# Optimization experiments

Measured on AMD Instinct MI355X. Metric: run time of the kernel, lower is better.

The kernel has to match this reference:

```python
import jax, jax.numpy as jnp
import numpy as np
from jax import lax

NUM_ITER = 20
STOP_THRESH = 1e-4
# kernels baked from anisotropy=(1,1,0.5): (3,3,3) and (max(1,int(3*s)),...)=(3,3,1)
KERNELS = ((3, 3, 3), (3, 3, 1))
LEAK = 0.01


def _maxpool3d(x, k):
    # x: [B,C,D,H,W]; stride 1, torch-style padding (k-1)//2 (pads with -inf for max)
    window = (1, 1) + k
    pad = [(0, 0), (0, 0)] + [((ki - 1) // 2, (ki - 1) // 2) for ki in k]
    return lax.reduce_window(x, -jnp.inf, lax.max, window, (1,) * 5, pad)


def soft_erode(img):
    p = [-_maxpool3d(-img, k) for k in KERNELS]
    return jnp.minimum(p[0], p[1])


def soft_dilate(img):
    p = [_maxpool3d(img, k) for k in KERNELS]
    return jnp.maximum(p[0], p[1])


def soft_open(img):
    return soft_dilate(soft_erode(img))


def _leaky(x):
    return jax.nn.leaky_relu(x, LEAK)


def soft_skel(img):
    skel = _leaky(img - soft_open(img))
    prev_skel = jnp.zeros_like(skel)
    active = jnp.array(True)  # emulates the data-dependent `break`
    for i in range(NUM_ITER):
        img = soft_erode(img)
        lr = 0.1 * 0.5 ** (i // (NUM_ITER // 5))
        delta = _leaky(img - soft_open(img))
        skel_update = _leaky(delta - skel * delta) * lr
        skel_new = skel + skel_update
        delta_norm = jnp.mean(jnp.abs(skel_new - prev_skel))
        # torch updates skel, THEN checks and breaks; freeze after stop triggers
        skel = jnp.where(active, skel_new, skel)
        active = jnp.logical_and(active, delta_norm >= STOP_THRESH)
        prev_skel = skel
    return skel


def distance_transform(x):
    binary = (x > 0).astype(x.dtype)
    return -1.0 * (1.0 - binary) * _maxpool3d(-binary, (3, 3, 3))


def setup_inputs() -> dict:
    key = jax.random.key(0)
    img = jax.random.uniform(key, (2, 1, 128, 256, 256), dtype=jnp.float32)
    return {"img": img}


def reference(img):
    skel = soft_skel(img)
    dt = distance_transform(lax.stop_gradient(skel))  # mirrors skel.detach()
    return skel * (1.0 + 0.2 * jax.nn.sigmoid(dt))
```

## Files before the change

kernel.cpp:

```cpp
#include <hip/hip_runtime.h>
#include <hip/hip_cooperative_groups.h>
#include <cmath>

#define D_ 128
#define H_ 256
#define W4 64
#define PS (H_*W4)
#define NTOT (2*128*256*256)
#define GBLK 2048
#define ROWS 8
#define TSTART 6
#define STOPF 1e-4f

typedef _Float16 h4 __attribute__((ext_vector_type(4)));
typedef _Float16 h2v __attribute__((ext_vector_type(2)));

__device__ __forceinline__ float lk(float x){ return x >= 0.f ? x : 0.01f*x; }
__device__ __forceinline__ float4 mn4(float4 a, float4 b){
    return make_float4(fminf(a.x,b.x),fminf(a.y,b.y),fminf(a.z,b.z),fminf(a.w,b.w)); }
__device__ __forceinline__ float4 ld4(const float4* p){ return *p; }
__device__ __forceinline__ float4 ld4(const h4* p){
    h4 v = *p; return make_float4((float)v.x,(float)v.y,(float)v.z,(float)v.w); }
__device__ __forceinline__ void st4(h4* p, float4 v){
    h4 r; r.x=(_Float16)v.x; r.y=(_Float16)v.y; r.z=(_Float16)v.z; r.w=(_Float16)v.w; *p = r; }
__device__ __forceinline__ float4 h4tof4(h4 v){
    return make_float4((float)v.x,(float)v.y,(float)v.z,(float)v.w); }

#define PINF 0x7C007C00u
#define NINF 0xFC00FC00u
__device__ __forceinline__ uint32_t pmin(uint32_t a, uint32_t b){
    h2v r = __builtin_elementwise_min(__builtin_bit_cast(h2v,a), __builtin_bit_cast(h2v,b));
    return __builtin_bit_cast(uint32_t, r); }
__device__ __forceinline__ uint32_t pmax(uint32_t a, uint32_t b){
    h2v r = __builtin_elementwise_max(__builtin_bit_cast(h2v,a), __builtin_bit_cast(h2v,b));
    return __builtin_bit_cast(uint32_t, r); }
__device__ __forceinline__ uint2 pmin2(uint2 a, uint2 b){
    return make_uint2(pmin(a.x,b.x), pmin(a.y,b.y)); }
__device__ __forceinline__ uint2 pmax2(uint2 a, uint2 b){
    return make_uint2(pmax(a.x,b.x), pmax(a.y,b.y)); }
__device__ __forceinline__ float4 cvt4(uint32_t w01, uint32_t w23){
    h2v a = __builtin_bit_cast(h2v, w01);
    h2v b = __builtin_bit_cast(h2v, w23);
    return make_float4((float)a.x, (float)a.y, (float)b.x, (float)b.y); }

struct Geo { int lane, h0; size_t pbase; bool pm, pp; };
__device__ __forceinline__ Geo mkgeo(int tid, int bi){
    Geo g;
    g.lane = tid & 63;
    int wv = tid >> 6;
    int q = bi & 7, d = (bi >> 3) & 127, b = bi >> 10;
    g.h0 = q*32 + wv*ROWS;
    g.pbase = ((size_t)(b*128 + d))*PS + (size_t)g.lane;
    g.pm = (d > 0); g.pp = (d < 127);
    return g;
}

__device__ __forceinline__ void phase_f32_erode(
    const float4* __restrict__ Xm, const float4* __restrict__ Xc, const float4* __restrict__ Xp,
    bool pm, bool pp, h4* __restrict__ Ep, int h0, int lane)
{
    const float INF = __builtin_inff();
    float4 dmn[4];
    auto ldrow = [&](int j){
        int s = j & 3; int h = h0 - 1 + j;
        if (h >= 0 && h < H_){
            float4 v = ld4(Xc + h*W4); float4 mn = v;
            if (pm){ mn = mn4(mn, ld4(Xm + h*W4)); }
            if (pp){ mn = mn4(mn, ld4(Xp + h*W4)); }
            dmn[s] = mn;
        } else dmn[s] = make_float4(INF,INF,INF,INF);
    };
    ldrow(0); ldrow(1); ldrow(2);
#pragma unroll
    for (int r = 0; r < ROWS; ++r){
        if (r + 3 <= ROWS + 1) ldrow(r+3);
        float4 vmn = mn4(dmn[r&3], mn4(dmn[(r+1)&3], dmn[(r+2)&3]));
        float lmn = __shfl_up(vmn.w,1);   if (lane == 0)  lmn = INF;
        float rmn = __shfl_down(vmn.x,1); if (lane == 63) rmn = INF;
        float4 e;
        e.x = fminf(lmn,  fminf(vmn.x,vmn.y));
        e.y = fminf(vmn.x,fminf(vmn.y,vmn.z));
        e.z = fminf(vmn.y,fminf(vmn.z,vmn.w));
        e.w = fminf(vmn.z,fminf(vmn.w,rmn));
        st4(Ep + (h0+r)*W4, e);
    }
}

template<int MODE, int R, typename CT>
__device__ __forceinline__ double phase_pk(
    const uint2* __restrict__ Xm, const uint2* __restrict__ Xc, const uint2* __restrict__ Xp,
    bool pm, bool pp,
    uint2* __restrict__ Ep, const CT* __restrict__ Cp, h4* __restrict__ Sp,
    float lr, int h0, int lane)
{
    uint2 rmn[4], rmx[4];
    double loc = 0.0;
    auto ldrow = [&](int j){
        int s = j & 3; int h = h0 - 1 + j;
        if (h >= 0 && h < H_){
            uint2 v = *(Xc + h*W4); uint2 mn = v, mx = v;
            if (pm){ uint2 u = *(Xm + h*W4); mn = pmin2(mn,u); mx = pmax2(mx,u); }
            if (pp){ uint2 u = *(Xp + h*W4); mn = pmin2(mn,u); mx = pmax2(mx,u); }
            rmn[s] = mn; rmx[s] = mx;
        } else {
            rmn[s] = make_uint2(PINF,PINF);
            rmx[s] = make_uint2(NINF,NINF);
        }
    };
    ldrow(0); ldrow(1); ldrow(2);
    float4 a_cur = ld4(Cp + h0*W4);
    float4 s_cur = make_float4(0,0,0,0);
    if constexpr(MODE >= 2) s_cur = ld4(Sp + h0*W4);
#pragma unroll
    for (int r = 0; r < R; ++r){
        if (r + 3 <= R + 1) ldrow(r+3);
        float4 a_nxt = a_cur, s_nxt = s_cur;
        if (r + 1 < R){
            a_nxt = ld4(Cp + (h0+r+1)*W4);
            if constexpr(MODE >= 2) s_nxt = ld4(Sp + (h0+r+1)*W4);
        }
        uint2 vmn = pmin2(rmn[r&3], pmin2(rmn[(r+1)&3], rmn[(r+2)&3]));
        uint2 vmx = pmax2(rmx[r&3], pmax2(rmx[(r+1)&3], rmx[(r+2)&3]));
        uint32_t pwn = __shfl_up(vmn.y,1);   if (lane == 0)  pwn = PINF;
        uint32_t nwn = __shfl_down(vmn.x,1); if (lane == 63) nwn = PINF;
        uint32_t l01 = (pwn  >> 16) | (vmn.x << 16);
        uint32_t l23 = (vmn.x >> 16) | (vmn.y << 16);
        uint32_t r23 = (vmn.y >> 16) | (nwn  << 16);
        uint32_t e01 = pmin(pmin(l01, vmn.x), l23);
        uint32_t e23 = pmin(pmin(l23, vmn.y), r23);
        *(Ep + (h0+r)*W4) = make_uint2(e01, e23);
        uint32_t pwx = __shfl_up(vmx.y,1);   if (lane == 0)  pwx = NINF;
        uint32_t nwx = __shfl_down(vmx.x,1); if (lane == 63) nwx = NINF;
        uint32_t L01 = (pwx  >> 16) | (vmx.x << 16);
        uint32_t L23 = (vmx.x >> 16) | (vmx.y << 16);
        uint32_t R23 = (vmx.y >> 16) | (nwx  << 16);
        uint32_t o01 = pmax(pmax(L01, vmx.x), L23);
        uint32_t o23 = pmax(pmax(L23, vmx.y), R23);
        float4 o = cvt4(o01, o23);
        float4 a = a_cur;
        if constexpr(MODE == 1){
            float4 s0;
            s0.x = lk(a.x-o.x); s0.y = lk(a.y-o.y);
            s0.z = lk(a.z-o.z); s0.w = lk(a.w-o.w);
            st4(Sp + (h0+r)*W4, s0);
        } else {
            float4 s = s_cur;
            float4 up; float dl;
            dl = lk(a.x-o.x); up.x = lk(dl - s.x*dl)*lr; s.x += up.x;
            dl = lk(a.y-o.y); up.y = lk(dl - s.y*dl)*lr; s.y += up.y;
            dl = lk(a.z-o.z); up.z = lk(dl - s.z*dl)*lr; s.z += up.z;
            dl = lk(a.w-o.w); up.w = lk(dl - s.w*dl)*lr; s.w += up.w;
            st4(Sp + (h0+r)*W4, s);
            if constexpr(MODE == 2)
                loc += (double)(fabsf(s.x)+fabsf(s.y)+fabsf(s.z)+fabsf(s.w));
            else
                loc += (double)(fabsf(up.x)+fabsf(up.y)+fabsf(up.z)+fabsf(up.w));
        }
        a_cur = a_nxt; s_cur = s_nxt;
    }
    return loc;
}

__global__ __launch_bounds__(256) void p0_k(const float* __restrict__ img0,
                                            h4* __restrict__ R0,
                                            int* __restrict__ frozen){
    if (blockIdx.x == 0 && threadIdx.x == 0) *frozen = 0;
    Geo g = mkgeo(threadIdx.x, blockIdx.x);
    const float4* Xc = (const float4*)img0 + g.pbase;
    phase_f32_erode(Xc-PS, Xc, Xc+PS, g.pm, g.pp, R0+g.pbase, g.h0, g.lane);
}

__global__ __launch_bounds__(256) void p1_k(const h4* __restrict__ R0,
                                            const float* __restrict__ img0,
                                            h4* __restrict__ R1,
                                            h4* __restrict__ S){
    Geo g = mkgeo(threadIdx.x, blockIdx.x);
    const uint2* Xc = (const uint2*)R0 + g.pbase;
    phase_pk<1,ROWS,float4>(Xc-PS, Xc, Xc+PS, g.pm, g.pp, (uint2*)R1 + g.pbase,
                            (const float4*)img0 + g.pbase, S + g.pbase, 0.f, g.h0, g.lane);
}

template<int MODE>
__global__ __launch_bounds__(256) void upd_k(const h4* __restrict__ Xb,
                                             const h4* __restrict__ Cb,
                                             h4* __restrict__ Eb,
                                             h4* __restrict__ Sb,
                                             const double* __restrict__ pr,
                                             double* __restrict__ pw,
                                             int* __restrict__ frozen,
                                             float* __restrict__ outp,
                                             float lr){
    if (*frozen) return;
    __shared__ double sm[4];
    int tid = threadIdx.x;
    int lane = tid & 63, wv = tid >> 6;
    if constexpr(MODE == 3){
        double v = 0.0;
#pragma unroll
        for (int j = 0; j < GBLK/256; ++j) v += pr[tid + 256*j];
#pragma unroll
        for (int o = 32; o; o >>= 1) v += __shfl_down(v, o);
        if (lane == 0) sm[wv] = v;
        __syncthreads();
        double tot = sm[0] + sm[1] + sm[2] + sm[3];
        if ((float)(tot / (double)NTOT) < STOPF){
            if (tid == 0) *frozen = 1;
            Geo g = mkgeo(tid, blockIdx.x);
            const h4* Sp = Sb + g.pbase;
            float4* O = (float4*)outp + g.pbase;
#pragma unroll
            for (int r = 0; r < ROWS; ++r){
                float4 s = h4tof4(Sp[(g.h0+r)*W4]);
                O[(g.h0+r)*W4] = make_float4(1.1f*s.x, 1.1f*s.y, 1.1f*s.z, 1.1f*s.w);
            }
            return;
        }
        __syncthreads();
    }
    Geo g = mkgeo(tid, blockIdx.x);
    const uint2* Xc = (const uint2*)Xb + g.pbase;
    double loc = phase_pk<MODE,ROWS,h4>(Xc-PS, Xc, Xc+PS, g.pm, g.pp,
                                        (uint2*)Eb + g.pbase, Cb + g.pbase, Sb + g.pbase,
                                        lr, g.h0, g.lane);
#pragma unroll
    for (int o = 32; o; o >>= 1) loc += __shfl_down(loc, o);
    if (lane == 0) sm[wv] = loc;
    __syncthreads();
    if (tid == 0) pw[blockIdx.x] = sm[0]+sm[1]+sm[2]+sm[3];
}

__global__ __launch_bounds__(256) void tail_k(h4* __restrict__ rg0,
                                              h4* __restrict__ rg1,
                                              h4* __restrict__ rg2,
                                              h4* __restrict__ S,
                                              float* __restrict__ outp,
                                              const double* __restrict__ pr0,
                                              double* __restrict__ tp0,
                                              double* __restrict__ tp1,
                                              const int* __restrict__ frozen){
    if (*frozen) return;
    cooperative_groups::grid_group gg = cooperative_groups::this_grid();
    __shared__ double sm[4];
    int tid = threadIdx.x, lane = tid & 63, wv = tid >> 6;
    int bi = blockIdx.x;
    int d = bi >> 3, b = (bi >> 2) & 1, q = bi & 3;
    int h0 = q*64 + wv*16;
    size_t pbase = ((size_t)(b*128 + d))*PS + (size_t)lane;
    bool pm = d > 0, pp = d < 127;
    const double* pr = pr0; int prn = GBLK;
    double* tpw = tp0;
    for (int i = TSTART; i < 20; ++i){
        double v = 0.0;
        for (int j = 0; j < prn/256; ++j) v += pr[tid + 256*j];
#pragma unroll
        for (int o = 32; o; o >>= 1) v += __shfl_down(v, o);
        if (lane == 0) sm[wv] = v;
        __syncthreads();
        double tot = sm[0] + sm[1] + sm[2] + sm[3];
        if ((float)(tot / (double)NTOT) < STOPF) break;
        __syncthreads();
        int xs = (i+1)%3, es = (i+2)%3, cs = i%3;
        h4* X = xs==0 ? rg0 : (xs==1 ? rg1 : rg2);
        h4* E = es==0 ? rg0 : (es==1 ? rg1 : rg2);
        h4* C = cs==0 ? rg0 : (cs==1 ? rg1 : rg2);
        float lr = 0.1f * exp2f(-(float)(i >> 2));
        const uint2* Xc = (const uint2*)X + pbase;
        double loc = phase_pk<3,16,h4>(Xc-PS, Xc, Xc+PS, pm, pp, (uint2*)E + pbase,
                                       C + pbase, S + pbase, lr, h0, lane);
#pragma unroll
        for (int o = 32; o; o >>= 1) loc += __shfl_down(loc, o);
        if (lane == 0) sm[wv] = loc;
        __syncthreads();
        if (tid == 0) tpw[blockIdx.x] = sm[0]+sm[1]+sm[2]+sm[3];
        gg.sync();
        pr = tpw; prn = 1024;
        tpw = (tpw == tp0) ? tp1 : tp0;
    }
    const h4* Sp = S + pbase;
    float4* O = (float4*)outp + pbase;
#pragma unroll
    for (int r = 0; r < 16; ++r){
        float4 s = h4tof4(Sp[(h0+r)*W4]);
        O[(h0+r)*W4] = make_float4(1.1f*s.x, 1.1f*s.y, 1.1f*s.z, 1.1f*s.w);
    }
}

__global__ __launch_bounds__(256) void scale_k(const h4* __restrict__ S,
                                               float* __restrict__ out){
    int t = blockIdx.x*256 + threadIdx.x;
#pragma unroll
    for (int c = 0; c < 4; ++c){
        int i = t + c*1048576;
        float4 s = ld4(S + i);
        float4 r = make_float4(1.1f*s.x, 1.1f*s.y, 1.1f*s.z, 1.1f*s.w);
        *(float4*)(out + (size_t)i*4) = r;
    }
}

extern "C" void kernel_launch(void* const* d_in, const int* in_sizes, int n_in,
                              void* d_out, int out_size, void* d_ws, size_t ws_size,
                              hipStream_t stream){
    const float* img0 = (const float*)d_in[0];
    float* out = (float*)d_out;
    char* ws = (char*)d_ws;
    size_t volh = (size_t)NTOT * 2;
    h4* ring[3] = { (h4*)ws, (h4*)(ws + volh), (h4*)(ws + 2*volh) };
    h4* S       = (h4*)(ws + 3*volh);
    double* parts[2] = { (double*)(ws + 4*volh), (double*)(ws + 4*volh) + GBLK };
    int* frozen = (int*)(ws + 4*volh + 2*GBLK*sizeof(double));
    double* tp0 = (double*)(ws + 4*volh + 2*GBLK*sizeof(double) + 256);
    double* tp1 = tp0 + 1024;

    dim3 blk(256), grd(GBLK);
    hipLaunchKernelGGL(p0_k, grd, blk, 0, stream, img0, ring[0], frozen);
    hipLaunchKernelGGL(p1_k, grd, blk, 0, stream, ring[0], img0, ring[1], S);

    for (int i = 0; i < TSTART; ++i){
        h4* C = ring[i % 3];
        h4* X = ring[(i+1) % 3];
        h4* E = ring[(i+2) % 3];
        float lr = (float)(0.1 * pow(0.5, (double)(i / 4)));
        double* pw = parts[i & 1];
        double* pr = parts[1 - (i & 1)];
        if (i == 0)
            hipLaunchKernelGGL((upd_k<2>), grd, blk, 0, stream, X, C, E, S, pr, pw, frozen, out, lr);
        else
            hipLaunchKernelGGL((upd_k<3>), grd, blk, 0, stream, X, C, E, S, pr, pw, frozen, out, lr);
    }

    h4* a_r0 = ring[0]; h4* a_r1 = ring[1]; h4* a_r2 = ring[2];
    h4* a_S = S; float* a_out = out;
    const double* a_pr0 = parts[1 - (TSTART & 1)];
    double* a_tp0 = tp0; double* a_tp1 = tp1; int* a_fz = frozen;
    void* args[9] = { &a_r0, &a_r1, &a_r2, &a_S, &a_out, &a_pr0, &a_tp0, &a_tp1, &a_fz };
    hipError_t ce = hipLaunchCooperativeKernel((const void*)tail_k, dim3(1024), blk,
                                               args, 0u, stream);
    if (ce != hipSuccess){
        for (int i = TSTART; i < 20; ++i){
            h4* C = ring[i % 3];
            h4* X = ring[(i+1) % 3];
            h4* E = ring[(i+2) % 3];
            float lr = (float)(0.1 * pow(0.5, (double)(i / 4)));
            double* pw = parts[i & 1];
            double* pr = parts[1 - (i & 1)];
            hipLaunchKernelGGL((upd_k<3>), grd, blk, 0, stream, X, C, E, S, pr, pw, frozen, out, lr);
        }
        hipLaunchKernelGGL(scale_k, dim3(4096), blk, 0, stream, S, out);
    }
}
```

Baseline: 289.7 us.

## Fuse two skeleton iterations per kernel with a two-level erosion stencil

Adds a new path in which each kernel advances two soft-skeleton iterations. It computes the second erosion and both opens from a depth-extended neighbourhood (d±2) loaded once, which roughly halves the number of launches and full-volume passes. Convergence norms are checked one pair late using per-iteration partial buffers, and the previous skeleton is kept so the output can come from the correct iterate. In exchange it does more redundant stencil work per pass, needs extra workspace, and only runs when the workspace is large enough; otherwise it falls back to the old cooperative path.

```diff
diff --git a/kernel.cpp b/kernel.cpp
--- a/kernel.cpp
+++ b/kernel.cpp
@@ -25,6 +25,8 @@
     h4 r; r.x=(_Float16)v.x; r.y=(_Float16)v.y; r.z=(_Float16)v.z; r.w=(_Float16)v.w; *p = r; }
 __device__ __forceinline__ float4 h4tof4(h4 v){
     return make_float4((float)v.x,(float)v.y,(float)v.z,(float)v.w); }
+__device__ __forceinline__ h4 f4toh4(float4 v){
+    h4 r; r.x=(_Float16)v.x; r.y=(_Float16)v.y; r.z=(_Float16)v.z; r.w=(_Float16)v.w; return r; }
 
 #define PINF 0x7C007C00u
 #define NINF 0xFC00FC00u
@@ -42,6 +44,25 @@
     h2v a = __builtin_bit_cast(h2v, w01);
     h2v b = __builtin_bit_cast(h2v, w23);
     return make_float4((float)a.x, (float)a.y, (float)b.x, (float)b.y); }
+__device__ __forceinline__ uint2 pk4(float4 v){
+    return __builtin_bit_cast(uint2, f4toh4(v)); }
+
+__device__ __forceinline__ uint2 hmin2(uint2 v, int lane){
+    uint32_t pw = __shfl_up(v.y,1);   if (lane == 0)  pw = PINF;
+    uint32_t nw = __shfl_down(v.x,1); if (lane == 63) nw = PINF;
+    uint32_t l01 = (pw  >> 16) | (v.x << 16);
+    uint32_t l23 = (v.x >> 16) | (v.y << 16);
+    uint32_t r23 = (v.y >> 16) | (nw  << 16);
+    return make_uint2(pmin(pmin(l01,v.x),l23), pmin(pmin(l23,v.y),r23));
+}
+__device__ __forceinline__ uint2 hmax2(uint2 v, int lane){
+    uint32_t pw = __shfl_up(v.y,1);   if (lane == 0)  pw = NINF;
+    uint32_t nw = __shfl_down(v.x,1); if (lane == 63) nw = NINF;
+    uint32_t l01 = (pw  >> 16) | (v.x << 16);
+    uint32_t l23 = (v.x >> 16) | (v.y << 16);
+    uint32_t r23 = (v.y >> 16) | (nw  << 16);
+    return make_uint2(pmax(pmax(l01,v.x),l23), pmax(pmax(l23,v.y),r23));
+}
 
 struct Geo { int lane, h0; size_t pbase; bool pm, pp; };
 __device__ __forceinline__ Geo mkgeo(int tid, int bi){
@@ -53,6 +74,267 @@
     g.pbase = ((size_t)(b*128 + d))*PS + (size_t)g.lane;
     g.pm = (d > 0); g.pp = (d < 127);
     return g;
+}
+
+__global__ __launch_bounds__(256) void init_k(const float* __restrict__ img0,
+                                              h4* __restrict__ R0,
+                                              h4* __restrict__ R1,
+                                              h4* __restrict__ Sb,
+                                              int* __restrict__ frozen){
+    if (blockIdx.x == 0 && threadIdx.x == 0) *frozen = 0;
+    int tid = threadIdx.x, lane = tid & 63, wv = tid >> 6;
+    int bi = blockIdx.x;
+    int q = bi & 7, d = (bi >> 3) & 127, b = bi >> 10;
+    int h0 = q*32 + wv*8;
+    size_t pbase = ((size_t)(b*128 + d))*PS + (size_t)lane;
+    bool dm1 = d >= 1, dm2 = d >= 2, dp1 = d <= 126, dp2 = d <= 125;
+    const float4* Xc = (const float4*)img0 + pbase;
+    uint2* E1w = (uint2*)R0 + pbase;
+    uint2* E2w = (uint2*)R1 + pbase;
+    h4*    Sw  = Sb + pbase;
+
+    float4 rawC[4];
+    uint2 mnA[4], mnB[4], mnC[4], mnE[4], mxE[4];
+
+    auto ldmg = [&](int h, int sl){
+        if (h >= 0 && h < H_){
+            const float4* p = Xc + h*W4;
+            float4 c4 = p[0]; rawC[sl] = c4;
+            uint2 c = pk4(c4);
+            uint2 xm1, xm2, xp1, xp2;
+            if (dm1) xm1 = pk4(p[-(int)PS]);
+            if (dm2) xm2 = pk4(p[-2*(int)PS]);
+            if (dp1) xp1 = pk4(p[(int)PS]);
+            if (dp2) xp2 = pk4(p[2*(int)PS]);
+            uint2 mb = c;
+            if (dm1) mb = pmin2(mb, xm1);
+            if (dp1) mb = pmin2(mb, xp1);
+            mnB[sl] = mb;
+            if (dm1){ uint2 a = pmin2(xm1, c); if (dm2) a = pmin2(a, xm2); mnA[sl] = a; }
+            if (dp1){ uint2 cc = pmin2(xp1, c); if (dp2) cc = pmin2(cc, xp2); mnC[sl] = cc; }
+        } else {
+            mnA[sl] = make_uint2(PINF,PINF); mnB[sl] = make_uint2(PINF,PINF);
+            mnC[sl] = make_uint2(PINF,PINF);
+            rawC[sl] = make_float4(0,0,0,0);
+        }
+    };
+    auto e1row = [&](int e, int s0, int s1, int s2, int se, bool wr){
+        if (e >= 0 && e < H_){
+            uint2 vb = pmin2(mnB[s0], pmin2(mnB[s1], mnB[s2]));
+            uint2 e1b = hmin2(vb, lane);
+            uint2 mn = e1b, mx = e1b;
+            if (dm1){
+                uint2 va = pmin2(mnA[s0], pmin2(mnA[s1], mnA[s2]));
+                uint2 e1a = hmin2(va, lane);
+                mn = pmin2(mn, e1a); mx = pmax2(mx, e1a);
+            }
+            if (dp1){
+                uint2 vc = pmin2(mnC[s0], pmin2(mnC[s1], mnC[s2]));
+                uint2 e1c = hmin2(vc, lane);
+                mn = pmin2(mn, e1c); mx = pmax2(mx, e1c);
+            }
+            mnE[se] = mn; mxE[se] = mx;
+            if (wr) E1w[e*W4] = e1b;
+        } else { mnE[se] = make_uint2(PINF,PINF); mxE[se] = make_uint2(NINF,NINF); }
+    };
+
+    ldmg(h0-2, 2); ldmg(h0-1, 3); ldmg(h0+0, 0); ldmg(h0+1, 1);
+    e1row(h0-1, 2,3,0, 3, false);
+    e1row(h0+0, 3,0,1, 0, true);
+#pragma unroll
+    for (int rr = 0; rr < 8; ++rr){
+        int r = h0 + rr;
+        ldmg(r+2, (rr+2)&3);
+        e1row(r+1, rr&3, (rr+1)&3, (rr+2)&3, (rr+1)&3, rr < 7);
+        uint2 v2 = pmin2(mnE[(rr+3)&3], pmin2(mnE[rr&3], mnE[(rr+1)&3]));
+        E2w[r*W4] = hmin2(v2, lane);
+        uint2 vv = pmax2(mxE[(rr+3)&3], pmax2(mxE[rr&3], mxE[(rr+1)&3]));
+        uint2 ow = hmax2(vv, lane);
+        float4 o = cvt4(ow.x, ow.y);
+        float4 a = rawC[rr&3];
+        float4 s0;
+        s0.x = lk(a.x-o.x); s0.y = lk(a.y-o.y);
+        s0.z = lk(a.z-o.z); s0.w = lk(a.w-o.w);
+        st4(Sw + r*W4, s0);
+    }
+}
+
+template<bool FIRST, bool P0>
+__global__ __launch_bounds__(256) void pair_k(const h4* __restrict__ Xb,
+                                              h4* CE1,
+                                              h4* __restrict__ E2b,
+                                              h4* __restrict__ Sb,
+                                              h4* __restrict__ Spb,
+                                              double* __restrict__ nA,
+                                              double* __restrict__ nB,
+                                              const double* __restrict__ g2,
+                                              const double* __restrict__ g1,
+                                              int* __restrict__ frozen,
+                                              float* __restrict__ outp,
+                                              float lr0, float lr1){
+    if (*frozen) return;
+    __shared__ double s2w[4], s1w[4], smA[4], smB[4];
+    int tid = threadIdx.x, lane = tid & 63, wv = tid >> 6;
+    int bi = blockIdx.x;
+    int q = bi & 7, d = (bi >> 3) & 127, b = bi >> 10;
+    int h0 = q*32 + wv*8;
+    size_t pbase = ((size_t)(b*128 + d))*PS + (size_t)lane;
+    if constexpr(!P0){
+        double v2 = 0.0, v1 = 0.0;
+#pragma unroll
+        for (int j = 0; j < GBLK/256; ++j){ v2 += g2[tid + 256*j]; v1 += g1[tid + 256*j]; }
+#pragma unroll
+        for (int o = 32; o; o >>= 1){ v2 += __shfl_down(v2,o); v1 += __shfl_down(v1,o); }
+        if (lane == 0){ s2w[wv] = v2; s1w[wv] = v1; }
+        __syncthreads();
+        double t2 = s2w[0]+s2w[1]+s2w[2]+s2w[3];
+        double t1 = s1w[0]+s1w[1]+s1w[2]+s1w[3];
+        bool f2 = (float)(t2 / (double)NTOT) < STOPF;
+        bool f1 = (float)(t1 / (double)NTOT) < STOPF;
+        if (f2 || f1){
+            if (tid == 0) *frozen = 1;
+            const h4* Sf = (f2 ? Spb : Sb) + pbase;
+            float4* O = (float4*)outp + pbase;
+#pragma unroll
+            for (int r = 0; r < 8; ++r){
+                float4 s = h4tof4(Sf[(h0+r)*W4]);
+                O[(h0+r)*W4] = make_float4(1.1f*s.x, 1.1f*s.y, 1.1f*s.z, 1.1f*s.w);
+            }
+            return;
+        }
+    }
+    bool dm1 = d >= 1, dm2 = d >= 2, dp1 = d <= 126, dp2 = d <= 125;
+    const uint2* Xc = (const uint2*)Xb + pbase;
+    const uint2* Cr = (const uint2*)CE1 + pbase;
+    uint2*       E1w = (uint2*)CE1 + pbase;
+    uint2*       E2w = (uint2*)E2b + pbase;
+    const uint2* Sr  = (const uint2*)Sb + pbase;
+    uint2*       Sw  = (uint2*)Sb + pbase;
+    uint2*       Spw = (uint2*)Spb + pbase;
+
+    uint2 rawC[4], mnA[4], mnB[4], mnC[4], mxB[4], mnE[4], mxE[4];
+    auto ldmg = [&](int h, int sl){
+        if (h >= 0 && h < H_){
+            const uint2* p = Xc + h*W4;
+            uint2 c = p[0]; rawC[sl] = c;
+            uint2 xm1, xm2, xp1, xp2;
+            if (dm1) xm1 = p[-(int)PS];
+            if (dm2) xm2 = p[-2*(int)PS];
+            if (dp1) xp1 = p[(int)PS];
+            if (dp2) xp2 = p[2*(int)PS];
+            uint2 mb = c, xb = c;
+            if (dm1){ mb = pmin2(mb, xm1); xb = pmax2(xb, xm1); }
+            if (dp1){ mb = pmin2(mb, xp1); xb = pmax2(xb, xp1); }
+            mnB[sl] = mb; mxB[sl] = xb;
+            if (dm1){ uint2 a = pmin2(xm1, c); if (dm2) a = pmin2(a, xm2); mnA[sl] = a; }
+            if (dp1){ uint2 cc = pmin2(xp1, c); if (dp2) cc = pmin2(cc, xp2); mnC[sl] = cc; }
+        } else {
+            mnA[sl] = make_uint2(PINF,PINF); mnB[sl] = make_uint2(PINF,PINF);
+            mnC[sl] = make_uint2(PINF,PINF); mxB[sl] = make_uint2(NINF,NINF);
+            rawC[sl] = make_uint2(0,0);
+        }
+    };
+    auto e1row = [&](int e, int s0, int s1, int s2, int se, bool wr){
+        if (e >= 0 && e < H_){
+            uint2 vb = pmin2(mnB[s0], pmin2(mnB[s1], mnB[s2]));
+            uint2 e1b = hmin2(vb, lane);
+            uint2 mn = e1b, mx = e1b;
+            if (dm1){
+                uint2 va = pmin2(mnA[s0], pmin2(mnA[s1], mnA[s2]));
+                uint2 e1a = hmin2(va, lane);
+                mn = pmin2(mn, e1a); mx = pmax2(mx, e1a);
+            }
+            if (dp1){
+                uint2 vc = pmin2(mnC[s0], pmin2(mnC[s1], mnC[s2]));
+                uint2 e1c = hmin2(vc, lane);
+                mn = pmin2(mn, e1c); mx = pmax2(mx, e1c);
+            }
+            mnE[se] = mn; mxE[se] = mx;
+            if (wr) E1w[e*W4] = e1b;
+        } else { mnE[se] = make_uint2(PINF,PINF); mxE[se] = make_uint2(NINF,NINF); }
+    };
+
+    ldmg(h0-2, 2); ldmg(h0-1, 3); ldmg(h0+0, 0); ldmg(h0+1, 1);
+    uint2 cw_cur = Cr[h0*W4];
+    uint2 s_cur  = Sr[h0*W4];
+    e1row(h0-1, 2,3,0, 3, false);
+    e1row(h0+0, 3,0,1, 0, true);
+    double locA = 0.0, locB = 0.0;
+#pragma unroll
+    for (int rr = 0; rr < 8; ++rr){
+        int r = h0 + rr;
+        uint2 cw_nxt = cw_cur, s_nxt = s_cur;
+        if (rr < 7){
+            cw_nxt = Cr[(r+1)*W4];
+            s_nxt  = Sr[(r+1)*W4];
+        }
+        ldmg(r+2, (rr+2)&3);
+        e1row(r+1, rr&3, (rr+1)&3, (rr+2)&3, (rr+1)&3, rr < 7);
+        uint2 v2 = pmin2(mnE[(rr+3)&3], pmin2(mnE[rr&3], mnE[(rr+1)&3]));
+        E2w[r*W4] = hmin2(v2, lane);
+        uint2 vv = pmax2(mxE[(rr+3)&3], pmax2(mxE[rr&3], mxE[(rr+1)&3]));
+        uint2 ovw = hmax2(vv, lane);
+        uint2 vi = pmax2(mxB[(rr+3)&3], pmax2(mxB[rr&3], mxB[(rr+1)&3]));
+        uint2 oiw = hmax2(vi, lane);
+        float4 o = cvt4(oiw.x, oiw.y);
+        float4 a = cvt4(cw_cur.x, cw_cur.y);
+        float4 s = cvt4(s_cur.x, s_cur.y);
+        float4 up; float dl;
+        dl = lk(a.x-o.x); up.x = lk(dl - s.x*dl)*lr0; s.x += up.x;
+        dl = lk(a.y-o.y); up.y = lk(dl - s.y*dl)*lr0; s.y += up.y;
+        dl = lk(a.z-o.z); up.z = lk(dl - s.z*dl)*lr0; s.z += up.z;
+        dl = lk(a.w-o.w); up.w = lk(dl - s.w*dl)*lr0; s.w += up.w;
+        if constexpr(FIRST)
+            locA += (double)(fabsf(s.x)+fabsf(s.y)+fabsf(s.z)+fabsf(s.w));
+        else
+            locA += (double)(fabsf(up.x)+fabsf(up.y)+fabsf(up.z)+fabsf(up.w));
+        h4 s1h = f4toh4(s);
+        Spw[r*W4] = __builtin_bit_cast(uint2, s1h);
+        float4 s2 = h4tof4(s1h);
+        float4 o1 = cvt4(ovw.x, ovw.y);
+        float4 a1 = cvt4(rawC[rr&3].x, rawC[rr&3].y);
+        dl = lk(a1.x-o1.x); up.x = lk(dl - s2.x*dl)*lr1; s2.x += up.x;
+        dl = lk(a1.y-o1.y); up.y = lk(dl - s2.y*dl)*lr1; s2.y += up.y;
+        dl = lk(a1.z-o1.z); up.z = lk(dl - s2.z*dl)*lr1; s2.z += up.z;
+        dl = lk(a1.w-o1.w); up.w = lk(dl - s2.w*dl)*lr1; s2.w += up.w;
+        locB += (double)(fabsf(up.x)+fabsf(up.y)+fabsf(up.z)+fabsf(up.w));
+        Sw[r*W4] = __builtin_bit_cast(uint2, f4toh4(s2));
+        cw_cur = cw_nxt; s_cur = s_nxt;
+    }
+#pragma unroll
+    for (int o = 32; o; o >>= 1){ locA += __shfl_down(locA,o); locB += __shfl_down(locB,o); }
+    if (lane == 0){ smA[wv] = locA; smB[wv] = locB; }
+    __syncthreads();
+    if (tid == 0){
+        nA[bi] = smA[0]+smA[1]+smA[2]+smA[3];
+        nB[bi] = smB[0]+smB[1]+smB[2]+smB[3];
+    }
+}
+
+__global__ __launch_bounds__(256) void finish_k(const h4* __restrict__ Sb,
+                                                const h4* __restrict__ Spb,
+                                                const double* __restrict__ g18,
+                                                const int* __restrict__ frozen,
+                                                float* __restrict__ outp){
+    if (*frozen) return;
+    __shared__ double sw[4];
+    int tid = threadIdx.x, lane = tid & 63, wv = tid >> 6;
+    double v = 0.0;
+#pragma unroll
+    for (int j = 0; j < GBLK/256; ++j) v += g18[tid + 256*j];
+#pragma unroll
+    for (int o = 32; o; o >>= 1) v += __shfl_down(v, o);
+    if (lane == 0) sw[wv] = v;
+    __syncthreads();
+    bool f18 = (float)((sw[0]+sw[1]+sw[2]+sw[3]) / (double)NTOT) < STOPF;
+    Geo g = mkgeo(tid, blockIdx.x);
+    const h4* Sf = (f18 ? Spb : Sb) + g.pbase;
+    float4* O = (float4*)outp + g.pbase;
+#pragma unroll
+    for (int r = 0; r < ROWS; ++r){
+        float4 s = h4tof4(Sf[(g.h0+r)*W4]);
+        O[(g.h0+r)*W4] = make_float4(1.1f*s.x, 1.1f*s.y, 1.1f*s.z, 1.1f*s.w);
+    }
 }
 
 __device__ __forceinline__ void phase_f32_erode(
@@ -121,22 +403,10 @@
         }
         uint2 vmn = pmin2(rmn[r&3], pmin2(rmn[(r+1)&3], rmn[(r+2)&3]));
         uint2 vmx = pmax2(rmx[r&3], pmax2(rmx[(r+1)&3], rmx[(r+2)&3]));
-        uint32_t pwn = __shfl_up(vmn.y,1);   if (lane == 0)  pwn = PINF;
-        uint32_t nwn = __shfl_down(vmn.x,1); if (lane == 63) nwn = PINF;
-        uint32_t l01 = (pwn  >> 16) | (vmn.x << 16);
-        uint32_t l23 = (vmn.x >> 16) | (vmn.y << 16);
-        uint32_t r23 = (vmn.y >> 16) | (nwn  << 16);
-        uint32_t e01 = pmin(pmin(l01, vmn.x), l23);
-        uint32_t e23 = pmin(pmin(l23, vmn.y), r23);
-        *(Ep + (h0+r)*W4) = make_uint2(e01, e23);
-        uint32_t pwx = __shfl_up(vmx.y,1);   if (lane == 0)  pwx = NINF;
-        uint32_t nwx = __shfl_down(vmx.x,1); if (lane == 63) nwx = NINF;
-        uint32_t L01 = (pwx  >> 16) | (vmx.x << 16);
-        uint32_t L23 = (vmx.x >> 16) | (vmx.y << 16);
-        uint32_t R23 = (vmx.y >> 16) | (nwx  << 16);
-        uint32_t o01 = pmax(pmax(L01, vmx.x), L23);
-        uint32_t o23 = pmax(pmax(L23, vmx.y), R23);
-        float4 o = cvt4(o01, o23);
+        uint2 ew = hmin2(vmn, lane);
+        *(Ep + (h0+r)*W4) = ew;
+        uint2 ow = hmax2(vmx, lane);
+        float4 o = cvt4(ow.x, ow.y);
         float4 a = a_cur;
         if constexpr(MODE == 1){
             float4 s0;
@@ -310,11 +580,40 @@
     int* frozen = (int*)(ws + 4*volh + 2*GBLK*sizeof(double));
     double* tp0 = (double*)(ws + 4*volh + 2*GBLK*sizeof(double) + 256);
     double* tp1 = tp0 + 1024;
+    h4* Sprev   = (h4*)(ws + 4*volh + 65536);
+    double* nrm = (double*)(ws + 4*volh + 65536 + volh);
+    size_t NEED = 4*volh + 65536 + volh + (size_t)20*GBLK*sizeof(double);
 
     dim3 blk(256), grd(GBLK);
+    if (ws_size >= NEED){
+        hipLaunchKernelGGL(init_k, grd, blk, 0, stream, img0, ring[0], ring[1], S, frozen);
+        for (int p = 0; p < 10; ++p){
+            h4* X  = (p & 1) ? ring[2] : ring[1];
+            h4* E2 = (p & 1) ? ring[1] : ring[2];
+            float l0 = (float)(0.1 * pow(0.5, (double)((2*p) / 4)));
+            float l1 = (float)(0.1 * pow(0.5, (double)((2*p+1) / 4)));
+            double* nA = nrm + (size_t)(2*p)   * GBLK;
+            double* nB = nrm + (size_t)(2*p+1) * GBLK;
+            if (p == 0){
+                hipLaunchKernelGGL((pair_k<true,true>), grd, blk, 0, stream,
+                                   X, ring[0], E2, S, Sprev, nA, nB,
+                                   (const double*)nullptr, (const double*)nullptr,
+                                   frozen, out, l0, l1);
+            } else {
+                const double* g2 = nrm + (size_t)(2*p-2) * GBLK;
+                const double* g1 = nrm + (size_t)(2*p-1) * GBLK;
+                hipLaunchKernelGGL((pair_k<false,false>), grd, blk, 0, stream,
+                                   X, ring[0], E2, S, Sprev, nA, nB,
+                                   g2, g1, frozen, out, l0, l1);
+            }
+        }
+        hipLaunchKernelGGL(finish_k, grd, blk, 0, stream,
+                           S, Sprev, nrm + (size_t)18*GBLK, frozen, out);
+        return;
+    }
+
     hipLaunchKernelGGL(p0_k, grd, blk, 0, stream, img0, ring[0], frozen);
     hipLaunchKernelGGL(p1_k, grd, blk, 0, stream, ring[0], img0, ring[1], S);
-
     for (int i = 0; i < TSTART; ++i){
         h4* C = ring[i % 3];
         h4* X = ring[(i+1) % 3];
@@ -327,7 +626,6 @@
         else
             hipLaunchKernelGGL((upd_k<3>), grd, blk, 0, stream, X, C, E, S, pr, pw, frozen, out, lr);
     }
-
     h4* a_r0 = ring[0]; h4* a_r1 = ring[1]; h4* a_r2 = ring[2];
     h4* a_S = S; float* a_out = out;
     const double* a_pr0 = parts[1 - (TSTART & 1)];
```

New measurement: 310.4 us. 7.1% more time.

## Fuse initial erode and first open/erode into one kernel; deepen row prefetch

Applied to the files above, without the earlier changes.

Replaces the two startup kernels (f32 erode, then packed erode+open producing the first skeleton) with a single init kernel. It reads the fp32 image with a wider depth halo (±2 planes) and recomputes the first erosion for neighbouring planes in registers, so it can write E1, E2 and the initial skeleton in one pass. This removes a kernel launch and a full round trip of the intermediate volume through global memory, at the cost of redundant min work and more registers. Separately, the shared phase routine now prefetches two input rows ahead and two C/S rows ahead, to hide memory latency better at the cost of extra register pressure.

```diff
diff --git a/kernel.cpp b/kernel.cpp
--- a/kernel.cpp
+++ b/kernel.cpp
@@ -16,8 +16,6 @@
 typedef _Float16 h2v __attribute__((ext_vector_type(2)));
 
 __device__ __forceinline__ float lk(float x){ return x >= 0.f ? x : 0.01f*x; }
-__device__ __forceinline__ float4 mn4(float4 a, float4 b){
-    return make_float4(fminf(a.x,b.x),fminf(a.y,b.y),fminf(a.z,b.z),fminf(a.w,b.w)); }
 __device__ __forceinline__ float4 ld4(const float4* p){ return *p; }
 __device__ __forceinline__ float4 ld4(const h4* p){
     h4 v = *p; return make_float4((float)v.x,(float)v.y,(float)v.z,(float)v.w); }
@@ -25,6 +23,8 @@
     h4 r; r.x=(_Float16)v.x; r.y=(_Float16)v.y; r.z=(_Float16)v.z; r.w=(_Float16)v.w; *p = r; }
 __device__ __forceinline__ float4 h4tof4(h4 v){
     return make_float4((float)v.x,(float)v.y,(float)v.z,(float)v.w); }
+__device__ __forceinline__ h4 f4toh4(float4 v){
+    h4 r; r.x=(_Float16)v.x; r.y=(_Float16)v.y; r.z=(_Float16)v.z; r.w=(_Float16)v.w; return r; }
 
 #define PINF 0x7C007C00u
 #define NINF 0xFC00FC00u
@@ -42,6 +42,25 @@
     h2v a = __builtin_bit_cast(h2v, w01);
     h2v b = __builtin_bit_cast(h2v, w23);
     return make_float4((float)a.x, (float)a.y, (float)b.x, (float)b.y); }
+__device__ __forceinline__ uint2 pk4(float4 v){
+    return __builtin_bit_cast(uint2, f4toh4(v)); }
+
+__device__ __forceinline__ uint2 hmin2(uint2 v, int lane){
+    uint32_t pw = __shfl_up(v.y,1);   if (lane == 0)  pw = PINF;
+    uint32_t nw = __shfl_down(v.x,1); if (lane == 63) nw = PINF;
+    uint32_t l01 = (pw  >> 16) | (v.x << 16);
+    uint32_t l23 = (v.x >> 16) | (v.y << 16);
+    uint32_t r23 = (v.y >> 16) | (nw  << 16);
+    return make_uint2(pmin(pmin(l01,v.x),l23), pmin(pmin(l23,v.y),r23));
+}
+__device__ __forceinline__ uint2 hmax2(uint2 v, int lane){
+    uint32_t pw = __shfl_up(v.y,1);   if (lane == 0)  pw = NINF;
+    uint32_t nw = __shfl_down(v.x,1); if (lane == 63) nw = NINF;
+    uint32_t l01 = (pw  >> 16) | (v.x << 16);
+    uint32_t l23 = (v.x >> 16) | (v.y << 16);
+    uint32_t r23 = (v.y >> 16) | (nw  << 16);
+    return make_uint2(pmax(pmax(l01,v.x),l23), pmax(pmax(l23,v.y),r23));
+}
 
 struct Geo { int lane, h0; size_t pbase; bool pm, pp; };
 __device__ __forceinline__ Geo mkgeo(int tid, int bi){
@@ -55,48 +74,100 @@
     return g;
 }
 
-__device__ __forceinline__ void phase_f32_erode(
-    const float4* __restrict__ Xm, const float4* __restrict__ Xc, const float4* __restrict__ Xp,
-    bool pm, bool pp, h4* __restrict__ Ep, int h0, int lane)
-{
-    const float INF = __builtin_inff();
-    float4 dmn[4];
-    auto ldrow = [&](int j){
-        int s = j & 3; int h = h0 - 1 + j;
+__global__ __launch_bounds__(256) void init_k(const float* __restrict__ img0,
+                                              h4* __restrict__ R0,
+                                              h4* __restrict__ R1,
+                                              h4* __restrict__ Sb,
+                                              int* __restrict__ frozen){
+    if (blockIdx.x == 0 && threadIdx.x == 0) *frozen = 0;
+    int tid = threadIdx.x, lane = tid & 63, wv = tid >> 6;
+    int bi = blockIdx.x;
+    int q = bi & 7, d = (bi >> 3) & 127, b = bi >> 10;
+    int h0 = q*32 + wv*8;
+    size_t pbase = ((size_t)(b*128 + d))*PS + (size_t)lane;
+    bool dm1 = d >= 1, dm2 = d >= 2, dp1 = d <= 126, dp2 = d <= 125;
+    const float4* Xc = (const float4*)img0 + pbase;
+    uint2* E1w = (uint2*)R0 + pbase;
+    uint2* E2w = (uint2*)R1 + pbase;
+    h4*    Sw  = Sb + pbase;
+
+    float4 rawC[4];
+    uint2 mnA[4], mnB[4], mnC[4], mnE[4], mxE[4];
+
+    auto ldmg = [&](int h, int sl){
         if (h >= 0 && h < H_){
-            float4 v = ld4(Xc + h*W4); float4 mn = v;
-            if (pm){ mn = mn4(mn, ld4(Xm + h*W4)); }
-            if (pp){ mn = mn4(mn, ld4(Xp + h*W4)); }
-            dmn[s] = mn;
-        } else dmn[s] = make_float4(INF,INF,INF,INF);
+            const float4* p = Xc + h*W4;
+            float4 c4 = p[0]; rawC[sl] = c4;
+            uint2 c = pk4(c4);
+            uint2 xm1, xm2, xp1, xp2;
+            if (dm1) xm1 = pk4(p[-(int)PS]);
+            if (dm2) xm2 = pk4(p[-2*(int)PS]);
+            if (dp1) xp1 = pk4(p[(int)PS]);
+            if (dp2) xp2 = pk4(p[2*(int)PS]);
+            uint2 mb = c;
+            if (dm1) mb = pmin2(mb, xm1);
+            if (dp1) mb = pmin2(mb, xp1);
+            mnB[sl] = mb;
+            if (dm1){ uint2 a = pmin2(xm1, c); if (dm2) a = pmin2(a, xm2); mnA[sl] = a; }
+            if (dp1){ uint2 cc = pmin2(xp1, c); if (dp2) cc = pmin2(cc, xp2); mnC[sl] = cc; }
+        } else {
+            mnA[sl] = make_uint2(PINF,PINF); mnB[sl] = make_uint2(PINF,PINF);
+            mnC[sl] = make_uint2(PINF,PINF);
+            rawC[sl] = make_float4(0,0,0,0);
+        }
     };
-    ldrow(0); ldrow(1); ldrow(2);
-#pragma unroll
-    for (int r = 0; r < ROWS; ++r){
-        if (r + 3 <= ROWS + 1) ldrow(r+3);
-        float4 vmn = mn4(dmn[r&3], mn4(dmn[(r+1)&3], dmn[(r+2)&3]));
-        float lmn = __shfl_up(vmn.w,1);   if (lane == 0)  lmn = INF;
-        float rmn = __shfl_down(vmn.x,1); if (lane == 63) rmn = INF;
-        float4 e;
-        e.x = fminf(lmn,  fminf(vmn.x,vmn.y));
-        e.y = fminf(vmn.x,fminf(vmn.y,vmn.z));
-        e.z = fminf(vmn.y,fminf(vmn.z,vmn.w));
-        e.w = fminf(vmn.z,fminf(vmn.w,rmn));
-        st4(Ep + (h0+r)*W4, e);
-    }
-}
-
-template<int MODE, int R, typename CT>
+    auto e1row = [&](int e, int s0, int s1, int s2, int se, bool wr){
+        if (e >= 0 && e < H_){
+            uint2 vb = pmin2(mnB[s0], pmin2(mnB[s1], mnB[s2]));
+            uint2 e1b = hmin2(vb, lane);
+            uint2 mn = e1b, mx = e1b;
+            if (dm1){
+                uint2 va = pmin2(mnA[s0], pmin2(mnA[s1], mnA[s2]));
+                uint2 e1a = hmin2(va, lane);
+                mn = pmin2(mn, e1a); mx = pmax2(mx, e1a);
+            }
+            if (dp1){
+                uint2 vc = pmin2(mnC[s0], pmin2(mnC[s1], mnC[s2]));
+                uint2 e1c = hmin2(vc, lane);
+                mn = pmin2(mn, e1c); mx = pmax2(mx, e1c);
+            }
+            mnE[se] = mn; mxE[se] = mx;
+            if (wr) E1w[e*W4] = e1b;
+        } else { mnE[se] = make_uint2(PINF,PINF); mxE[se] = make_uint2(NINF,NINF); }
+    };
+
+    ldmg(h0-2, 2); ldmg(h0-1, 3); ldmg(h0+0, 0); ldmg(h0+1, 1);
+    e1row(h0-1, 2,3,0, 3, false);
+    e1row(h0+0, 3,0,1, 0, true);
+#pragma unroll
+    for (int rr = 0; rr < 8; ++rr){
+        int r = h0 + rr;
+        ldmg(r+2, (rr+2)&3);
+        e1row(r+1, rr&3, (rr+1)&3, (rr+2)&3, (rr+1)&3, rr < 7);
+        uint2 v2 = pmin2(mnE[(rr+3)&3], pmin2(mnE[rr&3], mnE[(rr+1)&3]));
+        E2w[r*W4] = hmin2(v2, lane);
+        uint2 vv = pmax2(mxE[(rr+3)&3], pmax2(mxE[rr&3], mxE[(rr+1)&3]));
+        uint2 ow = hmax2(vv, lane);
+        float4 o = cvt4(ow.x, ow.y);
+        float4 a = rawC[rr&3];
+        float4 s0;
+        s0.x = lk(a.x-o.x); s0.y = lk(a.y-o.y);
+        s0.z = lk(a.z-o.z); s0.w = lk(a.w-o.w);
+        st4(Sw + r*W4, s0);
+    }
+}
+
+template<int MODE, int R>
 __device__ __forceinline__ double phase_pk(
     const uint2* __restrict__ Xm, const uint2* __restrict__ Xc, const uint2* __restrict__ Xp,
     bool pm, bool pp,
-    uint2* __restrict__ Ep, const CT* __restrict__ Cp, h4* __restrict__ Sp,
+    uint2* __restrict__ Ep, const h4* __restrict__ Cp, h4* __restrict__ Sp,
     float lr, int h0, int lane)
 {
-    uint2 rmn[4], rmx[4];
+    uint2 rmn[6], rmx[6];
     double loc = 0.0;
     auto ldrow = [&](int j){
-        int s = j & 3; int h = h0 - 1 + j;
+        int s = j % 6; int h = h0 - 1 + j;
         if (h >= 0 && h < H_){
             uint2 v = *(Xc + h*W4); uint2 mn = v, mx = v;
             if (pm){ uint2 u = *(Xm + h*W4); mn = pmin2(mn,u); mx = pmax2(mx,u); }
@@ -107,77 +178,39 @@
             rmx[s] = make_uint2(NINF,NINF);
         }
     };
-    ldrow(0); ldrow(1); ldrow(2);
-    float4 a_cur = ld4(Cp + h0*W4);
-    float4 s_cur = make_float4(0,0,0,0);
-    if constexpr(MODE >= 2) s_cur = ld4(Sp + h0*W4);
-#pragma unroll
-    for (int r = 0; r < R; ++r){
-        if (r + 3 <= R + 1) ldrow(r+3);
-        float4 a_nxt = a_cur, s_nxt = s_cur;
-        if (r + 1 < R){
-            a_nxt = ld4(Cp + (h0+r+1)*W4);
-            if constexpr(MODE >= 2) s_nxt = ld4(Sp + (h0+r+1)*W4);
-        }
-        uint2 vmn = pmin2(rmn[r&3], pmin2(rmn[(r+1)&3], rmn[(r+2)&3]));
-        uint2 vmx = pmax2(rmx[r&3], pmax2(rmx[(r+1)&3], rmx[(r+2)&3]));
-        uint32_t pwn = __shfl_up(vmn.y,1);   if (lane == 0)  pwn = PINF;
-        uint32_t nwn = __shfl_down(vmn.x,1); if (lane == 63) nwn = PINF;
-        uint32_t l01 = (pwn  >> 16) | (vmn.x << 16);
-        uint32_t l23 = (vmn.x >> 16) | (vmn.y << 16);
-        uint32_t r23 = (vmn.y >> 16) | (nwn  << 16);
-        uint32_t e01 = pmin(pmin(l01, vmn.x), l23);
-        uint32_t e23 = pmin(pmin(l23, vmn.y), r23);
-        *(Ep + (h0+r)*W4) = make_uint2(e01, e23);
-        uint32_t pwx = __shfl_up(vmx.y,1);   if (lane == 0)  pwx = NINF;
-        uint32_t nwx = __shfl_down(vmx.x,1); if (lane == 63) nwx = NINF;
-        uint32_t L01 = (pwx  >> 16) | (vmx.x << 16);
-        uint32_t L23 = (vmx.x >> 16) | (vmx.y << 16);
-        uint32_t R23 = (vmx.y >> 16) | (nwx  << 16);
-        uint32_t o01 = pmax(pmax(L01, vmx.x), L23);
-        uint32_t o23 = pmax(pmax(L23, vmx.y), R23);
-        float4 o = cvt4(o01, o23);
-        float4 a = a_cur;
-        if constexpr(MODE == 1){
-            float4 s0;
-            s0.x = lk(a.x-o.x); s0.y = lk(a.y-o.y);
-            s0.z = lk(a.z-o.z); s0.w = lk(a.w-o.w);
-            st4(Sp + (h0+r)*W4, s0);
-        } else {
-            float4 s = s_cur;
-            float4 up; float dl;
-            dl = lk(a.x-o.x); up.x = lk(dl - s.x*dl)*lr; s.x += up.x;
-            dl = lk(a.y-o.y); up.y = lk(dl - s.y*dl)*lr; s.y += up.y;
-            dl = lk(a.z-o.z); up.z = lk(dl - s.z*dl)*lr; s.z += up.z;
-            dl = lk(a.w-o.w); up.w = lk(dl - s.w*dl)*lr; s.w += up.w;
-            st4(Sp + (h0+r)*W4, s);
-            if constexpr(MODE == 2)
-                loc += (double)(fabsf(s.x)+fabsf(s.y)+fabsf(s.z)+fabsf(s.w));
-            else
-                loc += (double)(fabsf(up.x)+fabsf(up.y)+fabsf(up.z)+fabsf(up.w));
-        }
-        a_cur = a_nxt; s_cur = s_nxt;
+    ldrow(0); ldrow(1); ldrow(2); ldrow(3); ldrow(4);
+    float4 aC = ld4(Cp + h0*W4), aN1 = aC, aN2;
+    float4 sC = ld4(Sp + h0*W4), sN1 = sC, sN2;
+    if (R >= 2){ aN1 = ld4(Cp + (h0+1)*W4); sN1 = ld4(Sp + (h0+1)*W4); }
+#pragma unroll
+    for (int rr = 0; rr < R; ++rr){
+        if (rr + 5 <= R + 1) ldrow(rr+5);
+        aN2 = aN1; sN2 = sN1;
+        if (rr + 2 < R){
+            aN2 = ld4(Cp + (h0+rr+2)*W4);
+            sN2 = ld4(Sp + (h0+rr+2)*W4);
+        }
+        uint2 vmn = pmin2(rmn[rr%6], pmin2(rmn[(rr+1)%6], rmn[(rr+2)%6]));
+        uint2 vmx = pmax2(rmx[rr%6], pmax2(rmx[(rr+1)%6], rmx[(rr+2)%6]));
+        uint2 ew = hmin2(vmn, lane);
+        *(Ep + (h0+rr)*W4) = ew;
+        uint2 ow = hmax2(vmx, lane);
+        float4 o = cvt4(ow.x, ow.y);
+        float4 a = aC;
+        float4 s = sC;
+        float4 up; float dl;
+        dl = lk(a.x-o.x); up.x = lk(dl - s.x*dl)*lr; s.x += up.x;
+        dl = lk(a.y-o.y); up.y = lk(dl - s.y*dl)*lr; s.y += up.y;
+        dl = lk(a.z-o.z); up.z = lk(dl - s.z*dl)*lr; s.z += up.z;
+        dl = lk(a.w-o.w); up.w = lk(dl - s.w*dl)*lr; s.w += up.w;
+        st4(Sp + (h0+rr)*W4, s);
+        if constexpr(MODE == 2)
+            loc += (double)(fabsf(s.x)+fabsf(s.y)+fabsf(s.z)+fabsf(s.w));
+        else
+            loc += (double)(fabsf(up.x)+fabsf(up.y)+fabsf(up.z)+fabsf(up.w));
+        aC = aN1; sC = sN1; aN1 = aN2; sN1 = sN2;
     }
     return loc;
-}
-
-__global__ __launch_bounds__(256) void p0_k(const float* __restrict__ img0,
-                                            h4* __restrict__ R0,
-                                            int* __restrict__ frozen){
-    if (blockIdx.x == 0 && threadIdx.x == 0) *frozen = 0;
-    Geo g = mkgeo(threadIdx.x, blockIdx.x);
-    const float4* Xc = (const float4*)img0 + g.pbase;
-    phase_f32_erode(Xc-PS, Xc, Xc+PS, g.pm, g.pp, R0+g.pbase, g.h0, g.lane);
-}
-
-__global__ __launch_bounds__(256) void p1_k(const h4* __restrict__ R0,
-                                            const float* __restrict__ img0,
-                                            h4* __restrict__ R1,
-                                            h4* __restrict__ S){
-    Geo g = mkgeo(threadIdx.x, blockIdx.x);
-    const uint2* Xc = (const uint2*)R0 + g.pbase;
-    phase_pk<1,ROWS,float4>(Xc-PS, Xc, Xc+PS, g.pm, g.pp, (uint2*)R1 + g.pbase,
-                            (const float4*)img0 + g.pbase, S + g.pbase, 0.f, g.h0, g.lane);
 }
 
 template<int MODE>
@@ -219,9 +252,9 @@
     }
     Geo g = mkgeo(tid, blockIdx.x);
     const uint2* Xc = (const uint2*)Xb + g.pbase;
-    double loc = phase_pk<MODE,ROWS,h4>(Xc-PS, Xc, Xc+PS, g.pm, g.pp,
-                                        (uint2*)Eb + g.pbase, Cb + g.pbase, Sb + g.pbase,
-                                        lr, g.h0, g.lane);
+    double loc = phase_pk<MODE,ROWS>(Xc-PS, Xc, Xc+PS, g.pm, g.pp,
+                                     (uint2*)Eb + g.pbase, Cb + g.pbase, Sb + g.pbase,
+                                     lr, g.h0, g.lane);
 #pragma unroll
     for (int o = 32; o; o >>= 1) loc += __shfl_down(loc, o);
     if (lane == 0) sm[wv] = loc;
@@ -265,8 +298,8 @@
         h4* C = cs==0 ? rg0 : (cs==1 ? rg1 : rg2);
         float lr = 0.1f * exp2f(-(float)(i >> 2));
         const uint2* Xc = (const uint2*)X + pbase;
-        double loc = phase_pk<3,16,h4>(Xc-PS, Xc, Xc+PS, pm, pp, (uint2*)E + pbase,
-                                       C + pbase, S + pbase, lr, h0, lane);
+        double loc = phase_pk<3,16>(Xc-PS, Xc, Xc+PS, pm, pp, (uint2*)E + pbase,
+                                    C + pbase, S + pbase, lr, h0, lane);
 #pragma unroll
         for (int o = 32; o; o >>= 1) loc += __shfl_down(loc, o);
         if (lane == 0) sm[wv] = loc;
@@ -312,8 +345,7 @@
     double* tp1 = tp0 + 1024;
 
     dim3 blk(256), grd(GBLK);
-    hipLaunchKernelGGL(p0_k, grd, blk, 0, stream, img0, ring[0], frozen);
-    hipLaunchKernelGGL(p1_k, grd, blk, 0, stream, ring[0], img0, ring[1], S);
+    hipLaunchKernelGGL(init_k, grd, blk, 0, stream, img0, ring[0], ring[1], S, frozen);
 
     for (int i = 0; i < TSTART; ++i){
         h4* C = ring[i % 3];
```

Measured after the change: 300.7 us. +3.8%, slower.
